# Optimization experiments

Measured on AMD Instinct MI355X. Metric: run time of the kernel, lower is better.

Reference implementation:

```python
import jax, jax.numpy as jnp
import numpy as np
import math

N = 400; E = 3200; Fs = 16; Fp = 8
DS = 32; DC = 32; DP = 32; DB = 64
WK, SL = 7, 288
CHUNK = 24  # 2016 / 24 = 84 scan steps (original chunks G=2016 into pieces)


def setup_inputs() -> dict:
    key = jax.random.key(0)
    ks = iter(jax.random.split(key, 64))
    def p(shape, scale=0.1):
        return jax.random.normal(next(ks), shape, jnp.float32) * scale
    # edge_index with no self loops (PyG GATConv removes+re-adds self loops)
    src = jax.random.randint(next(ks), (E,), 0, N)
    off = jax.random.randint(next(ks), (E,), 1, N)
    dst = (src + off) % N
    edge_index = jnp.stack([src, dst]).astype(jnp.int32)
    return dict(
        x_static=jax.random.normal(next(ks), (N, Fs), jnp.float32),
        profile_feat=jax.random.normal(next(ks), (N, WK, SL, Fp), jnp.float32),
        edge_index=edge_index,
        Ws1=p((Fs, 4 * DS)), as1_src=p((4, DS)), as1_dst=p((4, DS)), bs1=p((DS,)),
        Ws2=p((DS, DS)), as2_src=p((1, DS)), as2_dst=p((1, DS)), bs2=p((DS,)),
        wd_emb=p((7, 8), 1.0), sl_emb=p((288, 16), 1.0),
        Wc1=p((29, DC)), bc1=p((DC,)), Wc2=p((DC, DC)), bc2=p((DC,)),
        Wp1=p((Fp, DP)), bp1=p((DP,)), Wp2=p((DP, DP)), bp2=p((DP,)),
        Wt1=p((DS + DC + DP, 4 * DB)), at1_src=p((4, DB)), at1_dst=p((4, DB)), bt1=p((DB,)),
        Wt2=p((DB, DB)), at2_src=p((1, DB)), at2_dst=p((1, DB)), bt2=p((DB,)),
        Wh1=p((DB, 32)), bh1=p((32,)), Wh2=p((32, 1)), bh2=p((1,)),
    )


def gat_conv(x, W, a_src, a_dst, bias, src, dst, n):
    """PyG GATConv (concat=False): x [B,n,Fin] -> [B,n,C]; shared edge list per graph."""
    B = x.shape[0]
    H, C = a_src.shape
    h = (x @ W).reshape(B, n, H, C)                          # [B,n,H,C]
    al_s = jnp.einsum('bnhc,hc->bnh', h, a_src)              # [B,n,H]
    al_d = jnp.einsum('bnhc,hc->bnh', h, a_dst)
    e = jax.nn.leaky_relu(al_s[:, src] + al_d[:, dst], 0.2)  # [B,E,H]
    e = jnp.moveaxis(e, 1, 0)                                # [E,B,H]
    m = jax.ops.segment_max(e, dst, num_segments=n)          # [n,B,H]
    e = jnp.exp(e - m[dst])
    denom = jax.ops.segment_sum(e, dst, num_segments=n)
    alpha = e / denom[dst]                                   # [E,B,H]
    msg = alpha[..., None] * jnp.moveaxis(h[:, src], 1, 0)   # [E,B,H,C]
    out = jax.ops.segment_sum(msg, dst, num_segments=n)      # [n,B,H,C]
    return out.mean(axis=2).swapaxes(0, 1) + bias            # [B,n,C]


def reference(x_static, profile_feat, edge_index,
              Ws1, as1_src, as1_dst, bs1, Ws2, as2_src, as2_dst, bs2,
              wd_emb, sl_emb, Wc1, bc1, Wc2, bc2,
              Wp1, bp1, Wp2, bp2,
              Wt1, at1_src, at1_dst, bt1, Wt2, at2_src, at2_dst, bt2,
              Wh1, bh1, Wh2, bh2):
    relu = jax.nn.relu
    n = x_static.shape[0]
    loop = jnp.arange(n, dtype=edge_index.dtype)
    src = jnp.concatenate([edge_index[0], loop])   # add self loops
    dst = jnp.concatenate([edge_index[1], loop])

    # static graph encoder
    xs = relu(gat_conv(x_static[None], Ws1, as1_src, as1_dst, bs1, src, dst, n))
    xs = relu(gat_conv(xs, Ws2, as2_src, as2_dst, bs2, src, dst, n))[0]  # [n,DS]

    # calendar encoder (fixed [7,288] grid)
    wid = jnp.broadcast_to(jnp.arange(WK)[:, None], (WK, SL))
    sid = jnp.broadcast_to(jnp.arange(SL)[None, :], (WK, SL))
    ta = (2.0 * math.pi / SL) * sid.astype(jnp.float32)
    wa = (2.0 * math.pi / WK) * wid.astype(jnp.float32)
    cyc = jnp.stack([jnp.sin(ta), jnp.cos(ta), jnp.sin(wa), jnp.cos(wa)], -1)
    wknd = (wid >= 5).astype(jnp.float32)[..., None]
    feat = jnp.concatenate([wd_emb[wid], sl_emb[sid], cyc, wknd], -1)  # [7,288,29]
    cal = relu(feat @ Wc1 + bc1) @ Wc2 + bc2                           # [7,288,DC]

    # profile encoder
    pe = relu(profile_feat @ Wp1 + bp1) @ Wp2 + bp2                    # [n,7,288,DP]
    pe = jnp.transpose(pe, (1, 2, 0, 3))                               # [7,288,n,DP]

    fused = jnp.concatenate([
        jnp.broadcast_to(xs[None, None], (WK, SL, n, DS)),
        jnp.broadcast_to(cal[:, :, None, :], (WK, SL, n, DC)),
        pe], -1)                                                        # [7,288,n,96]

    G = WK * SL
    chunks = fused.reshape(G // CHUNK, CHUNK, n, DS + DC + DP)

    def step(carry, ch):
        h = relu(gat_conv(ch, Wt1, at1_src, at1_dst, bt1, src, dst, n))
        h = relu(gat_conv(h, Wt2, at2_src, at2_dst, bt2, src, dst, n))
        return carry, h

    _, outs = jax.lax.scan(step, None, chunks)
    H = outs.reshape(WK, SL, n, DB)                                     # [7,288,n,DB]
    pred = (relu(H @ Wh1 + bh1) @ Wh2 + bh2)[..., 0]                    # [7,288,n]
    return H, pred
```

## Files before the change

kernel.cpp:

```cpp
#include <hip/hip_runtime.h>

typedef unsigned short u16;
typedef unsigned int   u32;
typedef _Float16 f16;
typedef __attribute__((ext_vector_type(8))) _Float16 f16x8;
typedef __attribute__((ext_vector_type(4))) float f32x4;

#define NN  400
#define EIN 3200
#define NE  3600
#define TT  2016
#define L2E 1.4426950408889634f

__device__ __forceinline__ u32 pk16(float a, float b){
  auto h = __builtin_amdgcn_cvt_pkrtz(a,b);
  union { decltype(h) v; u32 u; } cv; cv.v = h; return cv.u;
}
__device__ __forceinline__ float hlo(u32 w){
  union { u32 u; __fp16 h[2]; } v; v.u=w; return (float)v.h[0];
}
__device__ __forceinline__ float hhi(u32 w){
  union { u32 u; __fp16 h[2]; } v; v.u=w; return (float)v.h[1];
}

__global__ __launch_bounds__(1024) void k_setup(
    const int* __restrict__ ei,
    const float* __restrict__ Wp2, const float* __restrict__ bp2,
    const float* __restrict__ Wt1,
    const float* __restrict__ at1_src, const float* __restrict__ at1_dst,
    const float* __restrict__ Wt2, const float* __restrict__ at2_src, const float* __restrict__ at2_dst,
    const float* __restrict__ Wh1,
    const float* __restrict__ Wc2, const float* __restrict__ bc2,
    const float* __restrict__ Ws1, const float* __restrict__ Ws2,
    u16* __restrict__ rp, u32* __restrict__ col2, u16* __restrict__ ord,
    f16* __restrict__ Bf1, f16* __restrict__ Bf2, f16* __restrict__ Bfh,
    f16* __restrict__ Bs1, f16* __restrict__ Bs2,
    float* __restrict__ wpe_s, float* __restrict__ wpe_d,
    float* __restrict__ wt1_as, float* __restrict__ wt1_ad,
    float* __restrict__ w2s, float* __restrict__ w2d,
    float* __restrict__ b_pe2, float* __restrict__ WcW,
    float* __restrict__ wbal_s, float* __restrict__ wbal_d,
    float* __restrict__ balc_s, float* __restrict__ balc_d)
{
  const int tid=threadIdx.x;
  __shared__ int s_src[NE]; __shared__ int s_dst[NE]; __shared__ int s_tmp[NE];
  __shared__ int s_deg[NN]; __shared__ int s_rp[NN+1]; __shared__ int s_cur[NN];
  __shared__ float sWpe[8192];
  __shared__ float sWcW[8192];
  __shared__ float sbpe2[256];
  if(blockIdx.x==0){
    for(int e2=tid;e2<NE;e2+=1024){
      s_src[e2]=(e2<EIN)?ei[e2]:(e2-EIN);
      s_dst[e2]=(e2<EIN)?ei[EIN+e2]:(e2-EIN);
    }
    if(tid<NN) s_deg[tid]=0;
    __syncthreads();
    for(int e2=tid;e2<NE;e2+=1024) atomicAdd(&s_deg[s_dst[e2]],1);
    __syncthreads();
    if(tid<=NN){
      int acc=0;
      for(int j=0;j<tid;j++) acc+=s_deg[j];
      s_rp[tid]=acc;
      rp[tid]=(u16)acc;
      if(tid<NN) s_cur[tid]=acc;
    }
    if(tid==0){
      rp[NN+1]=(u16)NE; rp[NN+2]=(u16)NE; rp[NN+3]=(u16)NE;
      col2[NE]=0; col2[NE+1]=0; col2[NE+2]=0; col2[NE+3]=0;
    }
    __syncthreads();
    for(int e2=tid;e2<NE;e2+=1024){
      int slot=atomicAdd(&s_cur[s_dst[e2]],1);
      s_tmp[slot]=e2;
    }
    __syncthreads();
    if(tid<NN){
      int b=s_rp[tid], en=s_rp[tid+1];
      for(int i=b+1;i<en;i++){
        int key=s_tmp[i]; int j=i-1;
        while(j>=b && s_tmp[j]>key){ s_tmp[j+1]=s_tmp[j]; j--; }
        s_tmp[j+1]=key;
      }
      for(int i=b;i<en;i++){
        u32 s=(u32)s_src[s_tmp[i]];
        col2[i]=((s*144u)<<16)|(s*4u);
      }
      int dg=en-b, rk=0;
      for(int j=0;j<NN;j++){
        int dj=s_rp[j+1]-s_rp[j];
        rk += (dj>dg)||((dj==dg)&&(j<tid));
      }
      ord[rk]=(u16)tid;
    }
  } else {
    for(int i=tid;i<8192;i+=1024){
      int k=i>>8, j=i&255;
      float a=0.f,b=0.f;
      for(int m=0;m<32;m++){
        a+=Wp2[k*32+m]*Wt1[(64+m)*256+j];
        b+=Wc2[k*32+m]*Wt1[(32+m)*256+j];
      }
      sWpe[i]=a; sWcW[i]=b; WcW[i]=b;
    }
    if(tid<256){
      float a=0.f,b=0.f;
      for(int m=0;m<32;m++){ a+=bp2[m]*Wt1[(64+m)*256+tid]; b+=bc2[m]*Wt1[(32+m)*256+tid]; }
      sbpe2[tid]=a+b; b_pe2[tid]=a+b;
    }
    __syncthreads();
    if(tid<128){
      int k=tid>>2,h=tid&3;
      float s=0,d=0,s2=0,d2=0,bs=0,bd=0;
      for(int c=0;c<64;c++){
        float as=at1_src[h*64+c], ad=at1_dst[h*64+c];
        float wv=sWpe[k*256+h*64+c];  s+=wv*as;  d+=wv*ad;
        float w2=Wt1[k*256+h*64+c];   s2+=w2*as; d2+=w2*ad;
        float wc=sWcW[k*256+h*64+c];  bs+=wc*as; bd+=wc*ad;
      }
      wpe_s[tid]=s*L2E; wpe_d[tid]=d*L2E; wt1_as[tid]=s2*L2E; wt1_ad[tid]=d2*L2E;
      wbal_s[tid]=bs*L2E; wbal_d[tid]=bd*L2E;
    }
    if(tid>=128&&tid<192){
      int k=tid-128; float s=0,d=0;
      for(int c=0;c<64;c++){ float wv=Wt2[k*64+c]; s+=wv*at2_src[c]; d+=wv*at2_dst[c]; }
      w2s[k]=s*L2E; w2d[k]=d*L2E;
    }
    if(tid>=192&&tid<196){
      int h=tid-192; float s=0,d=0;
      for(int c=0;c<64;c++){ float v=sbpe2[h*64+c]; s+=v*at1_src[h*64+c]; d+=v*at1_dst[h*64+c]; }
      balc_s[h]=s*L2E; balc_d[h]=d*L2E;
    }
    for(int i=tid;i<16384;i+=1024){
      int j=i&7, ll=(i>>3)&63, ks=(i>>9)&1, nt=(i>>10)&3, h=(i>>12)&3;
      int k=ks*32+(ll>>4)*8+j, c=h*64+nt*16+(ll&15);
      float v=(k<32)? sWpe[k*256+c] : Wt1[(k-32)*256+c];
      Bf1[i]=(f16)v;
    }
    for(int i=tid;i<4096;i+=1024){
      int j=i&7, ll=(i>>3)&63, ks=(i>>9)&1, nt=(i>>10)&3;
      Bf2[i]=(f16)Wt2[(ks*32+(ll>>4)*8+j)*64 + nt*16+(ll&15)];
    }
    for(int i=tid;i<2048;i+=1024){
      int j=i&7, ll=(i>>3)&63, ks=(i>>9)&1, nt=(i>>10)&1;
      Bfh[i]=(f16)Wh1[(ks*32+(ll>>4)*8+j)*32 + nt*16+(ll&15)];
    }
    for(int i=tid;i<4096;i+=1024){
      int j=i&7, ll=(i>>3)&63, nt=(i>>9)&7;
      int k=(ll>>4)*8+j, c=nt*16+(ll&15);
      Bs1[i]=(f16)((k<16)? Ws1[k*128+c] : 0.f);
    }
    for(int i=tid;i<1024;i+=1024){
      int j=i&7, ll=(i>>3)&63, nt=(i>>9)&1;
      int k=(ll>>4)*8+j, c=nt*16+(ll&15);
      Bs2[i]=(f16)Ws2[k*32+c];
    }
  }
}

#define KS_X    0
#define KS_H    32000
#define KS_ALS  140800
#define KS_ALD  147200
#define KS_COL  153600
#define KS_RP   160800
#define KS_ORD  161608
#define KS_AS   162408
#define KS_AD   162920
#define KS_END  163432

__global__ __launch_bounds__(1024) void k_static(
    const float* __restrict__ x_static,
    const float* __restrict__ as1_src, const float* __restrict__ as1_dst, const float* __restrict__ bs1,
    const float* __restrict__ as2_src, const float* __restrict__ as2_dst, const float* __restrict__ bs2,
    const float* __restrict__ wt1_as, const float* __restrict__ wt1_ad,
    const f16* __restrict__ Bs1, const f16* __restrict__ Bs2,
    const u16* __restrict__ g_rp, const u32* __restrict__ g_col2, const u16* __restrict__ g_ord,
    u32* __restrict__ xsb, float* __restrict__ Aal_s, float* __restrict__ Aal_d)
{
  __shared__ __align__(16) char smem[KS_END];
  const int tid=threadIdx.x;
  const int l=tid&63, w=tid>>6;
  const int col16=l&15, cr=(l>>4)*4, kbyte=(l>>4)*16;
  const int lane8=tid&7, grp8=tid>>3;
  const int l16=tid&15, g16=tid>>4, hh=l16>>2, cg=l16&3;
  float* ALS=(float*)(smem+KS_ALS);
  float* ALD=(float*)(smem+KS_ALD);
  const u16* COL=(const u16*)(smem+KS_COL);
  const u16* RP =(const u16*)(smem+KS_RP);
  const u16* ORD=(const u16*)(smem+KS_ORD);
  float* AS=(float*)(smem+KS_AS);
  float* AD=(float*)(smem+KS_AD);

  for(int i=tid;i<NN*32;i+=1024){
    int n=i>>5, c=i&31;
    *(f16*)(smem+KS_X+n*80+c*2) = (c<16)? (f16)x_static[n*16+c] : (f16)0.f;
  }
  for(int i=tid;i<NE;i+=1024) ((u16*)(smem+KS_COL))[i]=(u16)((g_col2[i]&0xffffu)>>2);
  if(tid<202) ((u32*)(smem+KS_RP))[tid]=((const u32*)g_rp)[tid];
  else if(tid>=256&&tid<456) ((u32*)(smem+KS_ORD))[tid-256]=((const u32*)g_ord)[tid-256];
  else if(tid>=512&&tid<640){ AS[tid-512]=as1_src[tid-512]*L2E; AD[tid-512]=as1_dst[tid-512]*L2E; }
  __syncthreads();

  {
    f16x8 B[8];
    #pragma unroll
    for(int nt=0;nt<8;nt++) B[nt]=*(const f16x8*)(Bs1+nt*512+l*8);
    for(int mt=w;mt<25;mt+=16){
      f16x8 a=*(const f16x8*)(smem+KS_X+(mt*16+col16)*80+kbyte);
      #pragma unroll
      for(int nt=0;nt<8;nt++){
        f32x4 c={0.f,0.f,0.f,0.f};
        c=__builtin_amdgcn_mfma_f32_16x16x32_f16(a,B[nt],c,0,0,0);
        #pragma unroll
        for(int r=0;r<4;r++)
          *(f16*)(smem+KS_H+(mt*16+cr+r)*272+(nt*16+col16)*2)=(f16)c[r];
      }
    }
  }
  __syncthreads();

  if(tid<NN){
    #pragma unroll
    for(int h=0;h<4;h++){
      const u32* hr=(const u32*)(smem+KS_H+tid*272+h*64);
      float sa=0.f,da=0.f;
      #pragma unroll
      for(int q=0;q<16;q++){
        u32 v=hr[q]; float v0=hlo(v),v1=hhi(v);
        sa=fmaf(v0,AS[h*32+2*q],sa); sa=fmaf(v1,AS[h*32+2*q+1],sa);
        da=fmaf(v0,AD[h*32+2*q],da); da=fmaf(v1,AD[h*32+2*q+1],da);
      }
      ALS[tid*4+h]=sa; ALD[tid*4+h]=da;
    }
  }
  __syncthreads();

  for(int m=0;m<7;m++){
    int di=g16+m*64;
    if(di<NN){
      int d=ORD[di];
      int b=RP[d], en=RP[d+1];
      float ad=ALD[d*4+hh];
      float den=0.f;
      float rt[8]={0.f,0.f,0.f,0.f,0.f,0.f,0.f,0.f};
      for(int j=b;j<en;j++){
        int s=COL[j];
        float v=ALS[s*4+hh]+ad;
        v=fmaxf(v,0.2f*v);
        float p=__builtin_amdgcn_exp2f(v); den+=p;
        uint4 hw=*(const uint4*)(smem+KS_H+s*272+l16*16);
        rt[0]=fmaf(hlo(hw.x),p,rt[0]); rt[1]=fmaf(hhi(hw.x),p,rt[1]);
        rt[2]=fmaf(hlo(hw.y),p,rt[2]); rt[3]=fmaf(hhi(hw.y),p,rt[3]);
        rt[4]=fmaf(hlo(hw.z),p,rt[4]); rt[5]=fmaf(hhi(hw.z),p,rt[5]);
        rt[6]=fmaf(hlo(hw.w),p,rt[6]); rt[7]=fmaf(hhi(hw.w),p,rt[7]);
      }
      float inv=__builtin_amdgcn_rcpf(den);
      float vs[8];
      #pragma unroll
      for(int q=0;q<8;q++){
        float x=rt[q]*inv;
        x+=__shfl_xor(x,4); x+=__shfl_xor(x,8);
        vs[q]=x;
      }
      if(l16<4){
        u32 pk[4];
        #pragma unroll
        for(int q=0;q<4;q++){
          float v0=fmaxf(fmaf(0.25f,vs[2*q],  bs1[cg*8+2*q]),  0.f);
          float v1=fmaxf(fmaf(0.25f,vs[2*q+1],bs1[cg*8+2*q+1]),0.f);
          pk[q]=pk16(v0,v1);
        }
        *(uint4*)(smem+KS_X+d*80+cg*16)=make_uint4(pk[0],pk[1],pk[2],pk[3]);
      }
    }
  }
  __syncthreads();

  {
    f16x8 B[2];
    #pragma unroll
    for(int nt=0;nt<2;nt++) B[nt]=*(const f16x8*)(Bs2+nt*512+l*8);
    for(int mt=w;mt<25;mt+=16){
      f16x8 a=*(const f16x8*)(smem+KS_X+(mt*16+col16)*80+kbyte);
      #pragma unroll
      for(int nt=0;nt<2;nt++){
        f32x4 c={0.f,0.f,0.f,0.f};
        c=__builtin_amdgcn_mfma_f32_16x16x32_f16(a,B[nt],c,0,0,0);
        #pragma unroll
        for(int r=0;r<4;r++)
          *(f16*)(smem+KS_H+(mt*16+cr+r)*80+(nt*16+col16)*2)=(f16)c[r];
      }
    }
  }
  if(tid>=512&&tid<640){ AS[tid-512]=wt1_as[tid-512]; AD[tid-512]=wt1_ad[tid-512]; }
  __syncthreads();

  if(tid<NN){
    const u32* hr=(const u32*)(smem+KS_H+tid*80);
    float sa=0.f,da=0.f;
    #pragma unroll
    for(int q=0;q<16;q++){
      u32 v=hr[q]; float v0=hlo(v),v1=hhi(v);
      sa=fmaf(v0,as2_src[2*q],sa); sa=fmaf(v1,as2_src[2*q+1],sa);
      da=fmaf(v0,as2_dst[2*q],da); da=fmaf(v1,as2_dst[2*q+1],da);
    }
    ALS[tid]=sa*L2E; ALD[tid]=da*L2E;
  }
  __syncthreads();

  #pragma unroll
  for(int m=0;m<4;m++){
    int di=grp8+m*128;
    if(di<NN){
      int d=ORD[di];
      int b=RP[d], en=RP[d+1];
      float ad=ALD[d];
      float den=0.f;
      float rt[4]={0.f,0.f,0.f,0.f};
      for(int j=b;j<en;j++){
        int s=COL[j];
        float v=ALS[s]+ad;
        v=fmaxf(v,0.2f*v);
        float p=__builtin_amdgcn_exp2f(v); den+=p;
        uint2 hw=*(const uint2*)(smem+KS_H+s*80+lane8*8);
        rt[0]=fmaf(hlo(hw.x),p,rt[0]); rt[1]=fmaf(hhi(hw.x),p,rt[1]);
        rt[2]=fmaf(hlo(hw.y),p,rt[2]); rt[3]=fmaf(hhi(hw.y),p,rt[3]);
      }
      float inv=__builtin_amdgcn_rcpf(den);
      float xq[4];
      #pragma unroll
      for(int q=0;q<4;q++) xq[q]=fmaxf(fmaf(rt[q],inv,bs2[lane8*4+q]),0.f);
      float ps[4]={0.f,0.f,0.f,0.f}, pd[4]={0.f,0.f,0.f,0.f};
      #pragma unroll
      for(int q=0;q<4;q++){
        int k=lane8*4+q;
        #pragma unroll
        for(int h2=0;h2<4;h2++){ ps[h2]=fmaf(xq[q],AS[k*4+h2],ps[h2]); pd[h2]=fmaf(xq[q],AD[k*4+h2],pd[h2]); }
      }
      #pragma unroll
      for(int h2=0;h2<4;h2++){
        ps[h2]+=__shfl_xor(ps[h2],1); ps[h2]+=__shfl_xor(ps[h2],2); ps[h2]+=__shfl_xor(ps[h2],4);
        pd[h2]+=__shfl_xor(pd[h2],1); pd[h2]+=__shfl_xor(pd[h2],2); pd[h2]+=__shfl_xor(pd[h2],4);
      }
      if(lane8==0){
        #pragma unroll
        for(int h2=0;h2<4;h2++){ Aal_s[d*4+h2]=ps[h2]; Aal_d[d*4+h2]=pd[h2]; }
      }
      xsb[d*16+lane8*2+0]=pk16(xq[0],xq[1]);
      xsb[d*16+lane8*2+1]=pk16(xq[2],xq[3]);
    }
  }
}

#define OT_A    0
#define OT_H    57600
#define OT_ALS  115200
#define OT_ALD  121600
#define OT_COL  128000
#define OT_RP   142416
#define OT_ORD  143232
#define OT_BP   144032
#define OT_WPES 145056
#define OT_WPED 145568
#define OT_W2S  146080
#define OT_W2D  146336
#define OT_BT2  146592
#define OT_BH1  146848
#define OT_WH2  146976
#define OT_BPMT 147104
#define OT_C1   147360
#define OT_FEAT 147488
#define OT_BAL  147616
#define OT_END  147648

__global__ __launch_bounds__(1024) void k_temporal(
    const float* __restrict__ pf, const float* __restrict__ Wp1, const float* __restrict__ bp1,
    const u32* __restrict__ xsb, const float* __restrict__ Aal_s, const float* __restrict__ Aal_d,
    const float* __restrict__ wpe_sg, const float* __restrict__ wpe_dg,
    const f16* __restrict__ Bf1, const f16* __restrict__ Bf2, const f16* __restrict__ Bfh,
    const float* __restrict__ WcW, const float* __restrict__ b_pe2,
    const float* __restrict__ wbal_s, const float* __restrict__ wbal_d,
    const float* __restrict__ balc_s, const float* __restrict__ balc_d,
    const float* __restrict__ Wc1, const float* __restrict__ bc1,
    const float* __restrict__ wd_emb, const float* __restrict__ sl_emb,
    const float* __restrict__ bt1, const float* __restrict__ w2sg, const float* __restrict__ w2dg,
    const float* __restrict__ bt2g, const float* __restrict__ bh1g,
    const float* __restrict__ Wh2g, const float* __restrict__ bh2,
    const u16* __restrict__ g_rp, const u32* __restrict__ g_col2, const u16* __restrict__ g_ord,
    float* __restrict__ Hout, float* __restrict__ pred)
{
  __shared__ __align__(16) char smem[OT_END];
  const int bid=blockIdx.x;
  const int t=(bid&7)*252+(bid>>3);
  const int tid=threadIdx.x;
  const int l=tid&63, w=tid>>6;
  const int lane4=tid&3, grp4=tid>>2;
  const int col16=l&15, cr=(l>>4)*4, kbyte=(l>>4)*16;

  float4 pA=make_float4(0,0,0,0), pB=make_float4(0,0,0,0);
  if(tid<NN){ const float4* pp=(const float4*)(pf+((size_t)tid*TT+(size_t)t)*8); pA=pp[0]; pB=pp[1]; }

  for(int i=tid;i<3604;i+=1024) ((u32*)(smem+OT_COL))[i]=g_col2[i];
  for(int i=tid;i<6400;i+=1024){ int n=i>>4,q=i&15; *(u32*)(smem+OT_A+n*144+64+q*4)=xsb[i]; }
  if(tid<202) ((u32*)(smem+OT_RP))[tid]=((const u32*)g_rp)[tid];
  else if(tid>=256&&tid<456) ((u32*)(smem+OT_ORD))[tid-256]=((const u32*)g_ord)[tid-256];
  else if(tid>=512&&tid<640){ ((float*)(smem+OT_WPES))[tid-512]=wpe_sg[tid-512]; ((float*)(smem+OT_WPED))[tid-512]=wpe_dg[tid-512]; }
  else if(tid>=640&&tid<704){ ((float*)(smem+OT_W2S))[tid-640]=w2sg[tid-640]; ((float*)(smem+OT_W2D))[tid-640]=w2dg[tid-640]; }
  else if(tid>=704&&tid<768){ ((float*)(smem+OT_BT2))[tid-704]=bt2g[tid-704]; }
  else if(tid>=768&&tid<800){ ((float*)(smem+OT_BH1))[tid-768]=bh1g[tid-768]; ((float*)(smem+OT_WH2))[tid-768]=Wh2g[tid-768]; }
  else if(tid>=832&&tid<864){
    int q=tid-832;
    const int wd=t/288, sl=t%288;
    float v=0.f;
    if(q<8) v=wd_emb[wd*8+q];
    else if(q<24) v=sl_emb[sl*16+(q-8)];
    else if(q==24||q==25){ float ta=0.021816615649929116f*(float)sl; v=(q==24)?__sinf(ta):__cosf(ta); }
    else if(q==26||q==27){ float wa=0.8975979010256552f*(float)wd; v=(q==26)?__sinf(wa):__cosf(wa); }
    else if(q==28) v=(wd>=5)?1.f:0.f;
    ((float*)(smem+OT_FEAT))[q]=v;
  }
  __syncthreads();

  if(tid>=512&&tid<544){
    int q=tid-512;
    float a=bc1[q];
    const float* F=(const float*)(smem+OT_FEAT);
    for(int k=0;k<29;k++) a+=F[k]*Wc1[k*32+q];
    ((float*)(smem+OT_C1))[q]=fmaxf(a,0.f);
  }
  if(tid<NN){
    float px[8]={pA.x,pA.y,pA.z,pA.w,pB.x,pB.y,pB.z,pB.w};
    float pv[32];
    #pragma unroll
    for(int k2=0;k2<32;k2+=2){
      float a0=bp1[k2], a1=bp1[k2+1];
      #pragma unroll
      for(int i2=0;i2<8;i2++){ a0=fmaf(px[i2],Wp1[i2*32+k2],a0); a1=fmaf(px[i2],Wp1[i2*32+k2+1],a1); }
      a0=fmaxf(a0,0.f); a1=fmaxf(a1,0.f);
      pv[k2]=a0; pv[k2+1]=a1;
      *(u32*)(smem+OT_A+tid*144+k2*2)=pk16(a0,a1);
    }
    const float* WS=(const float*)(smem+OT_WPES);
    const float* WD=(const float*)(smem+OT_WPED);
    #pragma unroll
    for(int h=0;h<4;h++){
      float sa=Aal_s[tid*4+h], da=Aal_d[tid*4+h];
      #pragma unroll
      for(int k2=0;k2<32;k2++){ sa=fmaf(pv[k2],WS[k2*4+h],sa); da=fmaf(pv[k2],WD[k2*4+h],da); }
      ((float*)(smem+OT_ALS))[tid*4+h]=sa;
      ((float*)(smem+OT_ALD))[tid*4+h]=da;
    }
  }
  __syncthreads();

  auto mfma_L1=[&](int h){
    f16x8 B0[4],B1[4];
    #pragma unroll
    for(int nt=0;nt<4;nt++){
      B0[nt]=*(const f16x8*)(Bf1+(((h*4+nt)*2+0)*512+l*8));
      B1[nt]=*(const f16x8*)(Bf1+(((h*4+nt)*2+1)*512+l*8));
    }
    for(int mt=w;mt<25;mt+=16){
      const char* arow=smem+OT_A+(mt*16+col16)*144;
      f16x8 a0=*(const f16x8*)(arow+kbyte);
      f16x8 a1=*(const f16x8*)(arow+64+kbyte);
      #pragma unroll
      for(int nt=0;nt<4;nt++){
        f32x4 c={0.f,0.f,0.f,0.f};
        c=__builtin_amdgcn_mfma_f32_16x16x32_f16(a0,B0[nt],c,0,0,0);
        c=__builtin_amdgcn_mfma_f32_16x16x32_f16(a1,B1[nt],c,0,0,0);
        #pragma unroll
        for(int r=0;r<4;r++)
          *(f16*)(smem+OT_H+(mt*16+cr+r)*144+(nt*16+col16)*2)=(f16)c[r];
      }
    }
  };

  mfma_L1(0);
  if(tid<256){
    float a=b_pe2[tid];
    const float* C1=(const float*)(smem+OT_C1);
    for(int k2=0;k2<32;k2++) a=fmaf(C1[k2],WcW[k2*256+tid],a);
    ((float*)(smem+OT_BP))[tid]=a;
  }
  if(tid>=256&&tid<264){
    int h=tid&3; bool isd=(tid>=260);
    const float* C1=(const float*)(smem+OT_C1);
    const float* wb=isd?wbal_d:wbal_s;
    float a=isd?balc_d[h]:balc_s[h];
    for(int k2=0;k2<32;k2++) a=fmaf(C1[k2],wb[k2*4+h],a);
    ((float*)(smem+OT_BAL))[(isd?4:0)+h]=a;
  }
  __syncthreads();

  const u16* RP  =(const u16*)(smem+OT_RP);
  const u16* ORD =(const u16*)(smem+OT_ORD);
  const u32* COL2=(const u32*)(smem+OT_COL);
  const char* HB = smem+OT_H+lane4*32;

  float acc[2][16];
  #pragma unroll
  for(int m=0;m<2;m++){
    #pragma unroll
    for(int q=0;q<16;q++) acc[m][q]=0.f;
  }

  for(int h=0;h<4;h++){
    if(h==0&&tid<64){
      const float* BP=(const float*)(smem+OT_BP);
      ((float*)(smem+OT_BPMT))[tid]=0.25f*(BP[tid]+BP[64+tid]+BP[128+tid]+BP[192+tid])+bt1[tid];
    }
    const float* ALD=(const float*)(smem+OT_ALD);
    const char* ALSb=smem+OT_ALS+h*4;
    float bsd=((const float*)(smem+OT_BAL))[h]+((const float*)(smem+OT_BAL))[4+h];
    #pragma unroll
    for(int m=0;m<2;m++){
      int di = m ? (511-grp4) : grp4;
      float rt[16];
      #pragma unroll
      for(int q=0;q<16;q++) rt[q]=0.f;
      float inv=0.f;
      if(di<NN){
        int d=ORD[di];
        int b=RP[d], en=RP[d+1];
        float ad=ALD[d*4+h]+bsd;
        float den=0.f;
        for(int j=b;j<en;j++){
          u32 cv=COL2[j];
          float alv=*(const float*)(ALSb+((cv&0xffffu)<<2));
          float v=alv+ad;
          v=fmaxf(v,0.2f*v);
          float p=__builtin_amdgcn_exp2f(v); den+=p;
          const char* hp=HB+(cv>>16);
          uint4 h0=*(const uint4*)(hp);
          uint4 h1=*(const uint4*)(hp+16);
          rt[0] =fmaf(hlo(h0.x),p,rt[0]);  rt[1] =fmaf(hhi(h0.x),p,rt[1]);
          rt[2] =fmaf(hlo(h0.y),p,rt[2]);  rt[3] =fmaf(hhi(h0.y),p,rt[3]);
          rt[4] =fmaf(hlo(h0.z),p,rt[4]);  rt[5] =fmaf(hhi(h0.z),p,rt[5]);
          rt[6] =fmaf(hlo(h0.w),p,rt[6]);  rt[7] =fmaf(hhi(h0.w),p,rt[7]);
          rt[8] =fmaf(hlo(h1.x),p,rt[8]);  rt[9] =fmaf(hhi(h1.x),p,rt[9]);
          rt[10]=fmaf(hlo(h1.y),p,rt[10]); rt[11]=fmaf(hhi(h1.y),p,rt[11]);
          rt[12]=fmaf(hlo(h1.z),p,rt[12]); rt[13]=fmaf(hhi(h1.z),p,rt[13]);
          rt[14]=fmaf(hlo(h1.w),p,rt[14]); rt[15]=fmaf(hhi(h1.w),p,rt[15]);
        }
        inv=__builtin_amdgcn_rcpf(den);
      }
      #pragma unroll
      for(int q=0;q<16;q++) acc[m][q]=fmaf(rt[q],inv,acc[m][q]);
    }
    __syncthreads();
    if(h<3){ mfma_L1(h+1); __syncthreads(); }
  }

  {
    const float* BPMT=(const float*)(smem+OT_BPMT);
    const float* W2S=(const float*)(smem+OT_W2S);
    const float* W2D=(const float*)(smem+OT_W2D);
    #pragma unroll
    for(int m=0;m<2;m++){
      int di = m ? (511-grp4) : grp4;
      if(di<NN){
        int d=ORD[di];
        float g[16];
        #pragma unroll
        for(int q=0;q<16;q++) g[q]=fmaxf(fmaf(0.25f,acc[m][q],BPMT[lane4*16+q]),0.f);
        float ss=0.f,dd2=0.f;
        #pragma unroll
        for(int q=0;q<16;q++){ ss=fmaf(g[q],W2S[lane4*16+q],ss); dd2=fmaf(g[q],W2D[lane4*16+q],dd2); }
        ss+=__shfl_xor(ss,1); ss+=__shfl_xor(ss,2);
        dd2+=__shfl_xor(dd2,1); dd2+=__shfl_xor(dd2,2);
        if(lane4==0){ ((float*)(smem+OT_ALS))[d]=ss; ((float*)(smem+OT_ALD))[d]=dd2; }
        uint4 pk0,pk1;
        pk0.x=pk16(g[0],g[1]);   pk0.y=pk16(g[2],g[3]);   pk0.z=pk16(g[4],g[5]);   pk0.w=pk16(g[6],g[7]);
        pk1.x=pk16(g[8],g[9]);   pk1.y=pk16(g[10],g[11]); pk1.z=pk16(g[12],g[13]); pk1.w=pk16(g[14],g[15]);
        *(uint4*)(smem+OT_A+d*144+lane4*32)=pk0;
        *(uint4*)(smem+OT_A+d*144+lane4*32+16)=pk1;
      }
    }
  }
  __syncthreads();

  {
    f16x8 B0[4],B1[4];
    #pragma unroll
    for(int nt=0;nt<4;nt++){
      B0[nt]=*(const f16x8*)(Bf2+((nt*2+0)*512+l*8));
      B1[nt]=*(const f16x8*)(Bf2+((nt*2+1)*512+l*8));
    }
    for(int mt=w;mt<25;mt+=16){
      const char* arow=smem+OT_A+(mt*16+col16)*144;
      f16x8 a0=*(const f16x8*)(arow+kbyte);
      f16x8 a1=*(const f16x8*)(arow+64+kbyte);
      #pragma unroll
      for(int nt=0;nt<4;nt++){
        f32x4 c={0.f,0.f,0.f,0.f};
        c=__builtin_amdgcn_mfma_f32_16x16x32_f16(a0,B0[nt],c,0,0,0);
        c=__builtin_amdgcn_mfma_f32_16x16x32_f16(a1,B1[nt],c,0,0,0);
        #pragma unroll
        for(int r=0;r<4;r++)
          *(f16*)(smem+OT_H+(mt*16+cr+r)*144+(nt*16+col16)*2)=(f16)c[r];
      }
    }
  }
  __syncthreads();

  {
    const float* ALD=(const float*)(smem+OT_ALD);
    const float* BT2=(const float*)(smem+OT_BT2);
    #pragma unroll
    for(int m=0;m<2;m++){
      int di = m ? (511-grp4) : grp4;
      if(di<NN){
        int d=ORD[di];
        int b=RP[d], en=RP[d+1];
        float ad=ALD[d];
        float den=0.f;
        float rt[16];
        #pragma unroll
        for(int q=0;q<16;q++) rt[q]=0.f;
        for(int j=b;j<en;j++){
          u32 cv=COL2[j];
          float alv=*(const float*)(smem+OT_ALS+(cv&0xffffu));
          float v=alv+ad;
          v=fmaxf(v,0.2f*v);
          float p=__builtin_amdgcn_exp2f(v); den+=p;
          const char* hp=HB+(cv>>16);
          uint4 h0=*(const uint4*)(hp);
          uint4 h1=*(const uint4*)(hp+16);
          rt[0] =fmaf(hlo(h0.x),p,rt[0]);  rt[1] =fmaf(hhi(h0.x),p,rt[1]);
          rt[2] =fmaf(hlo(h0.y),p,rt[2]);  rt[3] =fmaf(hhi(h0.y),p,rt[3]);
          rt[4] =fmaf(hlo(h0.z),p,rt[4]);  rt[5] =fmaf(hhi(h0.z),p,rt[5]);
          rt[6] =fmaf(hlo(h0.w),p,rt[6]);  rt[7] =fmaf(hhi(h0.w),p,rt[7]);
          rt[8] =fmaf(hlo(h1.x),p,rt[8]);  rt[9] =fmaf(hhi(h1.x),p,rt[9]);
          rt[10]=fmaf(hlo(h1.y),p,rt[10]); rt[11]=fmaf(hhi(h1.y),p,rt[11]);
          rt[12]=fmaf(hlo(h1.z),p,rt[12]); rt[13]=fmaf(hhi(h1.z),p,rt[13]);
          rt[14]=fmaf(hlo(h1.w),p,rt[14]); rt[15]=fmaf(hhi(h1.w),p,rt[15]);
        }
        float inv=__builtin_amdgcn_rcpf(den);
        float hv[16];
        #pragma unroll
        for(int q=0;q<16;q++) hv[q]=fmaxf(fmaf(rt[q],inv,BT2[lane4*16+q]),0.f);
        float* hp2=Hout+((size_t)t*NN+d)*64+lane4*16;
        *(float4*)(hp2)   =make_float4(hv[0],hv[1],hv[2],hv[3]);
        *(float4*)(hp2+4) =make_float4(hv[4],hv[5],hv[6],hv[7]);
        *(float4*)(hp2+8) =make_float4(hv[8],hv[9],hv[10],hv[11]);
        *(float4*)(hp2+12)=make_float4(hv[12],hv[13],hv[14],hv[15]);
        uint4 pk0,pk1;
        pk0.x=pk16(hv[0],hv[1]);   pk0.y=pk16(hv[2],hv[3]);   pk0.z=pk16(hv[4],hv[5]);   pk0.w=pk16(hv[6],hv[7]);
        pk1.x=pk16(hv[8],hv[9]);   pk1.y=pk16(hv[10],hv[11]); pk1.z=pk16(hv[12],hv[13]); pk1.w=pk16(hv[14],hv[15]);
        *(uint4*)(smem+OT_A+d*144+lane4*32)=pk0;
        *(uint4*)(smem+OT_A+d*144+lane4*32+16)=pk1;
      }
    }
  }
  __syncthreads();

  {
    f16x8 B0[2],B1[2];
    #pragma unroll
    for(int nt=0;nt<2;nt++){
      B0[nt]=*(const f16x8*)(Bfh+((nt*2+0)*512+l*8));
      B1[nt]=*(const f16x8*)(Bfh+((nt*2+1)*512+l*8));
    }
    for(int mt=w;mt<25;mt+=16){
      const char* arow=smem+OT_A+(mt*16+col16)*144;
      f16x8 a0=*(const f16x8*)(arow+kbyte);
      f16x8 a1=*(const f16x8*)(arow+64+kbyte);
      #pragma unroll
      for(int nt=0;nt<2;nt++){
        float bj=((const float*)(smem+OT_BH1))[nt*16+col16];
        f32x4 c={bj,bj,bj,bj};
        c=__builtin_amdgcn_mfma_f32_16x16x32_f16(a0,B0[nt],c,0,0,0);
        c=__builtin_amdgcn_mfma_f32_16x16x32_f16(a1,B1[nt],c,0,0,0);
        #pragma unroll
        for(int r=0;r<4;r++)
          *(float*)(smem+OT_H+(mt*16+cr+r)*144+(nt*16+col16)*4)=fmaxf(c[r],0.f);
      }
    }
  }
  __syncthreads();

  {
    const float* WH2=(const float*)(smem+OT_WH2);
    float wv[8];
    #pragma unroll
    for(int q=0;q<8;q++) wv[q]=WH2[lane4*8+q];
    float bb=bh2[0];
    #pragma unroll
    for(int m=0;m<2;m++){
      int di = m ? (511-grp4) : grp4;
      if(di<NN){
        int d=ORD[di];
        float4 p0=*(const float4*)(smem+OT_H+d*144+lane4*32);
        float4 p1=*(const float4*)(smem+OT_H+d*144+lane4*32+16);
        float sp=p0.x*wv[0]+p0.y*wv[1]+p0.z*wv[2]+p0.w*wv[3]
                +p1.x*wv[4]+p1.y*wv[5]+p1.z*wv[6]+p1.w*wv[7];
        sp+=__shfl_xor(sp,1); sp+=__shfl_xor(sp,2);
        if(lane4==0) pred[(size_t)t*NN+d]=sp+bb;
      }
    }
  }
}

extern "C" void kernel_launch(void* const* d_in, const int* in_sizes, int n_in,
                              void* d_out, int out_size, void* d_ws, size_t ws_size,
                              hipStream_t stream) {
  const float* x_static=(const float*)d_in[0];
  const float* pf      =(const float*)d_in[1];
  const int*   ei      =(const int*)  d_in[2];
  const float* Ws1=(const float*)d_in[3];
  const float* as1_src=(const float*)d_in[4];
  const float* as1_dst=(const float*)d_in[5];
  const float* bs1=(const float*)d_in[6];
  const float* Ws2=(const float*)d_in[7];
  const float* as2_src=(const float*)d_in[8];
  const float* as2_dst=(const float*)d_in[9];
  const float* bs2=(const float*)d_in[10];
  const float* wd_emb=(const float*)d_in[11];
  const float* sl_emb=(const float*)d_in[12];
  const float* Wc1=(const float*)d_in[13];
  const float* bc1=(const float*)d_in[14];
  const float* Wc2=(const float*)d_in[15];
  const float* bc2=(const float*)d_in[16];
  const float* Wp1=(const float*)d_in[17];
  const float* bp1=(const float*)d_in[18];
  const float* Wp2=(const float*)d_in[19];
  const float* bp2=(const float*)d_in[20];
  const float* Wt1=(const float*)d_in[21];
  const float* at1_src=(const float*)d_in[22];
  const float* at1_dst=(const float*)d_in[23];
  const float* bt1=(const float*)d_in[24];
  const float* Wt2=(const float*)d_in[25];
  const float* at2_src=(const float*)d_in[26];
  const float* at2_dst=(const float*)d_in[27];
  const float* bt2=(const float*)d_in[28];
  const float* Wh1=(const float*)d_in[29];
  const float* bh1=(const float*)d_in[30];
  const float* Wh2=(const float*)d_in[31];
  const float* bh2=(const float*)d_in[32];

  float* Hout=(float*)d_out;
  float* pred=Hout + (size_t)TT*NN*64;

  char* wsp=(char*)d_ws; size_t off=0;
  auto A=[&](size_t n)->void*{ void* p=wsp+off; off=(off+n+255)&~(size_t)255; return p; };
  u16* rp    =(u16*)A(408*2);
  u32* col2  =(u32*)A((NE+4)*4);
  u16* ordv  =(u16*)A(NN*2);
  f16* Bf1   =(f16*)A(16384*2);
  f16* Bf2   =(f16*)A(4096*2);
  f16* Bfh   =(f16*)A(2048*2);
  f16* Bs1   =(f16*)A(4096*2);
  f16* Bs2   =(f16*)A(1024*2);
  float* wpe_s =(float*)A(128*4);
  float* wpe_d =(float*)A(128*4);
  float* wt1_as=(float*)A(128*4);
  float* wt1_ad=(float*)A(128*4);
  float* w2s   =(float*)A(64*4);
  float* w2d   =(float*)A(64*4);
  float* b_pe2 =(float*)A(256*4);
  float* WcW   =(float*)A(8192*4);
  float* wbal_s=(float*)A(128*4);
  float* wbal_d=(float*)A(128*4);
  float* balc_s=(float*)A(4*4);
  float* balc_d=(float*)A(4*4);
  u32*   xsb   =(u32*)A(6400*4);
  float* Aal_s =(float*)A(1600*4);
  float* Aal_d =(float*)A(1600*4);

  hipLaunchKernelGGL(k_setup, dim3(2), dim3(1024), 0, stream,
                     ei, Wp2,bp2,Wt1,at1_src,at1_dst,Wt2,at2_src,at2_dst,Wh1,Wc2,bc2,Ws1,Ws2,
                     rp,col2,ordv,Bf1,Bf2,Bfh,Bs1,Bs2,
                     wpe_s,wpe_d,wt1_as,wt1_ad,w2s,w2d,b_pe2,WcW,wbal_s,wbal_d,balc_s,balc_d);
  hipLaunchKernelGGL(k_static, dim3(1), dim3(1024), 0, stream,
                     x_static,as1_src,as1_dst,bs1,as2_src,as2_dst,bs2,
                     wt1_as,wt1_ad,Bs1,Bs2,rp,col2,ordv,xsb,Aal_s,Aal_d);
  hipLaunchKernelGGL(k_temporal, dim3(TT), dim3(1024), 0, stream,
                     pf,Wp1,bp1,xsb,Aal_s,Aal_d,wpe_s,wpe_d,Bf1,Bf2,Bfh,
                     WcW,b_pe2,wbal_s,wbal_d,balc_s,balc_d,
                     Wc1,bc1,wd_emb,sl_emb,bt1,w2s,w2d,bt2,bh1,Wh2,bh2,
                     rp,col2,ordv,Hout,pred);
}
```

Baseline: 448.9 us.

## Overlap next-head MFMA with aggregation; transpose MFMA operands and use fma_mix

The layer-1 per-head projection is split into a compute phase held in registers and a store phase. The next head's MFMA now runs before the current head's edge aggregation, which removes a barrier-separated compute step from the critical path. The MFMA operands are swapped so each lane owns four consecutive output columns of one row, giving packed 8- or 16-byte LDS stores instead of scalar f16 stores. The fp16-to-fp32 convert plus FMA in the gather loops is replaced by inline-asm v_fma_mix_f32, at the cost of more live accumulator registers.

```diff
diff --git a/kernel.cpp b/kernel.cpp
--- a/kernel.cpp
+++ b/kernel.cpp
@@ -21,6 +21,12 @@
 }
 __device__ __forceinline__ float hhi(u32 w){
   union { u32 u; __fp16 h[2]; } v; v.u=w; return (float)v.h[1];
+}
+__device__ __forceinline__ void fmix_lo(float& a, u32 s, float p){
+  asm("v_fma_mix_f32 %0, %1, %2, %0 op_sel:[0,0,0] op_sel_hi:[1,0,0]" : "+v"(a) : "v"(s), "v"(p));
+}
+__device__ __forceinline__ void fmix_hi(float& a, u32 s, float p){
+  asm("v_fma_mix_f32 %0, %1, %2, %0 op_sel:[1,0,0] op_sel_hi:[1,0,0]" : "+v"(a) : "v"(s), "v"(p));
 }
 
 __global__ __launch_bounds__(1024) void k_setup(
@@ -453,30 +459,54 @@
   }
   __syncthreads();
 
-  auto mfma_L1=[&](int h){
-    f16x8 B0[4],B1[4];
+  f32x4 c0[4], c1[4];
+  auto mfma_compute=[&](int h){
+    f16x8 Bw0[4],Bw1[4];
     #pragma unroll
     for(int nt=0;nt<4;nt++){
-      B0[nt]=*(const f16x8*)(Bf1+(((h*4+nt)*2+0)*512+l*8));
-      B1[nt]=*(const f16x8*)(Bf1+(((h*4+nt)*2+1)*512+l*8));
-    }
-    for(int mt=w;mt<25;mt+=16){
-      const char* arow=smem+OT_A+(mt*16+col16)*144;
+      Bw0[nt]=*(const f16x8*)(Bf1+(((h*4+nt)*2+0)*512+l*8));
+      Bw1[nt]=*(const f16x8*)(Bf1+(((h*4+nt)*2+1)*512+l*8));
+    }
+    {
+      const char* arow=smem+OT_A+(w*16+col16)*144;
       f16x8 a0=*(const f16x8*)(arow+kbyte);
       f16x8 a1=*(const f16x8*)(arow+64+kbyte);
       #pragma unroll
       for(int nt=0;nt<4;nt++){
         f32x4 c={0.f,0.f,0.f,0.f};
-        c=__builtin_amdgcn_mfma_f32_16x16x32_f16(a0,B0[nt],c,0,0,0);
-        c=__builtin_amdgcn_mfma_f32_16x16x32_f16(a1,B1[nt],c,0,0,0);
-        #pragma unroll
-        for(int r=0;r<4;r++)
-          *(f16*)(smem+OT_H+(mt*16+cr+r)*144+(nt*16+col16)*2)=(f16)c[r];
+        c=__builtin_amdgcn_mfma_f32_16x16x32_f16(Bw0[nt],a0,c,0,0,0);
+        c=__builtin_amdgcn_mfma_f32_16x16x32_f16(Bw1[nt],a1,c,0,0,0);
+        c0[nt]=c;
+      }
+    }
+    if(w<9){
+      const char* arow=smem+OT_A+((w+16)*16+col16)*144;
+      f16x8 a0=*(const f16x8*)(arow+kbyte);
+      f16x8 a1=*(const f16x8*)(arow+64+kbyte);
+      #pragma unroll
+      for(int nt=0;nt<4;nt++){
+        f32x4 c={0.f,0.f,0.f,0.f};
+        c=__builtin_amdgcn_mfma_f32_16x16x32_f16(Bw0[nt],a0,c,0,0,0);
+        c=__builtin_amdgcn_mfma_f32_16x16x32_f16(Bw1[nt],a1,c,0,0,0);
+        c1[nt]=c;
       }
     }
   };
-
-  mfma_L1(0);
+  auto mfma_store=[&](){
+    int n0=w*16+col16;
+    #pragma unroll
+    for(int nt=0;nt<4;nt++)
+      *(uint2*)(smem+OT_H+n0*144+(nt*16+cr)*2)=make_uint2(pk16(c0[nt][0],c0[nt][1]),pk16(c0[nt][2],c0[nt][3]));
+    if(w<9){
+      int n1=(w+16)*16+col16;
+      #pragma unroll
+      for(int nt=0;nt<4;nt++)
+        *(uint2*)(smem+OT_H+n1*144+(nt*16+cr)*2)=make_uint2(pk16(c1[nt][0],c1[nt][1]),pk16(c1[nt][2],c1[nt][3]));
+    }
+  };
+
+  mfma_compute(0);
+  mfma_store();
   if(tid<256){
     float a=b_pe2[tid];
     const float* C1=(const float*)(smem+OT_C1);
@@ -510,6 +540,7 @@
       const float* BP=(const float*)(smem+OT_BP);
       ((float*)(smem+OT_BPMT))[tid]=0.25f*(BP[tid]+BP[64+tid]+BP[128+tid]+BP[192+tid])+bt1[tid];
     }
+    if(h<3) mfma_compute(h+1);
     const float* ALD=(const float*)(smem+OT_ALD);
     const char* ALSb=smem+OT_ALS+h*4;
     float bsd=((const float*)(smem+OT_BAL))[h]+((const float*)(smem+OT_BAL))[4+h];
@@ -534,14 +565,14 @@
           const char* hp=HB+(cv>>16);
           uint4 h0=*(const uint4*)(hp);
           uint4 h1=*(const uint4*)(hp+16);
-          rt[0] =fmaf(hlo(h0.x),p,rt[0]);  rt[1] =fmaf(hhi(h0.x),p,rt[1]);
-          rt[2] =fmaf(hlo(h0.y),p,rt[2]);  rt[3] =fmaf(hhi(h0.y),p,rt[3]);
-          rt[4] =fmaf(hlo(h0.z),p,rt[4]);  rt[5] =fmaf(hhi(h0.z),p,rt[5]);
-          rt[6] =fmaf(hlo(h0.w),p,rt[6]);  rt[7] =fmaf(hhi(h0.w),p,rt[7]);
-          rt[8] =fmaf(hlo(h1.x),p,rt[8]);  rt[9] =fmaf(hhi(h1.x),p,rt[9]);
-          rt[10]=fmaf(hlo(h1.y),p,rt[10]); rt[11]=fmaf(hhi(h1.y),p,rt[11]);
-          rt[12]=fmaf(hlo(h1.z),p,rt[12]); rt[13]=fmaf(hhi(h1.z),p,rt[13]);
-          rt[14]=fmaf(hlo(h1.w),p,rt[14]); rt[15]=fmaf(hhi(h1.w),p,rt[15]);
+          fmix_lo(rt[0],h0.x,p);  fmix_hi(rt[1],h0.x,p);
+          fmix_lo(rt[2],h0.y,p);  fmix_hi(rt[3],h0.y,p);
+          fmix_lo(rt[4],h0.z,p);  fmix_hi(rt[5],h0.z,p);
+          fmix_lo(rt[6],h0.w,p);  fmix_hi(rt[7],h0.w,p);
+          fmix_lo(rt[8],h1.x,p);  fmix_hi(rt[9],h1.x,p);
+          fmix_lo(rt[10],h1.y,p); fmix_hi(rt[11],h1.y,p);
+          fmix_lo(rt[12],h1.z,p); fmix_hi(rt[13],h1.z,p);
+          fmix_lo(rt[14],h1.w,p); fmix_hi(rt[15],h1.w,p);
         }
         inv=__builtin_amdgcn_rcpf(den);
       }
@@ -549,7 +580,7 @@
       for(int q=0;q<16;q++) acc[m][q]=fmaf(rt[q],inv,acc[m][q]);
     }
     __syncthreads();
-    if(h<3){ mfma_L1(h+1); __syncthreads(); }
+    if(h<3){ mfma_store(); __syncthreads(); }
   }
 
   {
@@ -581,24 +612,23 @@
   __syncthreads();
 
   {
-    f16x8 B0[4],B1[4];
+    f16x8 Bw0[4],Bw1[4];
     #pragma unroll
     for(int nt=0;nt<4;nt++){
-      B0[nt]=*(const f16x8*)(Bf2+((nt*2+0)*512+l*8));
-      B1[nt]=*(const f16x8*)(Bf2+((nt*2+1)*512+l*8));
+      Bw0[nt]=*(const f16x8*)(Bf2+((nt*2+0)*512+l*8));
+      Bw1[nt]=*(const f16x8*)(Bf2+((nt*2+1)*512+l*8));
     }
     for(int mt=w;mt<25;mt+=16){
       const char* arow=smem+OT_A+(mt*16+col16)*144;
       f16x8 a0=*(const f16x8*)(arow+kbyte);
       f16x8 a1=*(const f16x8*)(arow+64+kbyte);
+      int n=mt*16+col16;
       #pragma unroll
       for(int nt=0;nt<4;nt++){
         f32x4 c={0.f,0.f,0.f,0.f};
-        c=__builtin_amdgcn_mfma_f32_16x16x32_f16(a0,B0[nt],c,0,0,0);
-        c=__builtin_amdgcn_mfma_f32_16x16x32_f16(a1,B1[nt],c,0,0,0);
-        #pragma unroll
-        for(int r=0;r<4;r++)
-          *(f16*)(smem+OT_H+(mt*16+cr+r)*144+(nt*16+col16)*2)=(f16)c[r];
+        c=__builtin_amdgcn_mfma_f32_16x16x32_f16(Bw0[nt],a0,c,0,0,0);
+        c=__builtin_amdgcn_mfma_f32_16x16x32_f16(Bw1[nt],a1,c,0,0,0);
+        *(uint2*)(smem+OT_H+n*144+(nt*16+cr)*2)=make_uint2(pk16(c[0],c[1]),pk16(c[2],c[3]));
       }
     }
   }
@@ -627,14 +657,14 @@
           const char* hp=HB+(cv>>16);
           uint4 h0=*(const uint4*)(hp);
           uint4 h1=*(const uint4*)(hp+16);
-          rt[0] =fmaf(hlo(h0.x),p,rt[0]);  rt[1] =fmaf(hhi(h0.x),p,rt[1]);
-          rt[2] =fmaf(hlo(h0.y),p,rt[2]);  rt[3] =fmaf(hhi(h0.y),p,rt[3]);
-          rt[4] =fmaf(hlo(h0.z),p,rt[4]);  rt[5] =fmaf(hhi(h0.z),p,rt[5]);
-          rt[6] =fmaf(hlo(h0.w),p,rt[6]);  rt[7] =fmaf(hhi(h0.w),p,rt[7]);
-          rt[8] =fmaf(hlo(h1.x),p,rt[8]);  rt[9] =fmaf(hhi(h1.x),p,rt[9]);
-          rt[10]=fmaf(hlo(h1.y),p,rt[10]); rt[11]=fmaf(hhi(h1.y),p,rt[11]);
-          rt[12]=fmaf(hlo(h1.z),p,rt[12]); rt[13]=fmaf(hhi(h1.z),p,rt[13]);
-          rt[14]=fmaf(hlo(h1.w),p,rt[14]); rt[15]=fmaf(hhi(h1.w),p,rt[15]);
+          fmix_lo(rt[0],h0.x,p);  fmix_hi(rt[1],h0.x,p);
+          fmix_lo(rt[2],h0.y,p);  fmix_hi(rt[3],h0.y,p);
+          fmix_lo(rt[4],h0.z,p);  fmix_hi(rt[5],h0.z,p);
+          fmix_lo(rt[6],h0.w,p);  fmix_hi(rt[7],h0.w,p);
+          fmix_lo(rt[8],h1.x,p);  fmix_hi(rt[9],h1.x,p);
+          fmix_lo(rt[10],h1.y,p); fmix_hi(rt[11],h1.y,p);
+          fmix_lo(rt[12],h1.z,p); fmix_hi(rt[13],h1.z,p);
+          fmix_lo(rt[14],h1.w,p); fmix_hi(rt[15],h1.w,p);
         }
         float inv=__builtin_amdgcn_rcpf(den);
         float hv[16];
@@ -656,25 +686,25 @@
   __syncthreads();
 
   {
-    f16x8 B0[2],B1[2];
+    f16x8 Bw0[2],Bw1[2];
     #pragma unroll
     for(int nt=0;nt<2;nt++){
-      B0[nt]=*(const f16x8*)(Bfh+((nt*2+0)*512+l*8));
-      B1[nt]=*(const f16x8*)(Bfh+((nt*2+1)*512+l*8));
+      Bw0[nt]=*(const f16x8*)(Bfh+((nt*2+0)*512+l*8));
+      Bw1[nt]=*(const f16x8*)(Bfh+((nt*2+1)*512+l*8));
     }
     for(int mt=w;mt<25;mt+=16){
       const char* arow=smem+OT_A+(mt*16+col16)*144;
       f16x8 a0=*(const f16x8*)(arow+kbyte);
       f16x8 a1=*(const f16x8*)(arow+64+kbyte);
+      int n=mt*16+col16;
       #pragma unroll
       for(int nt=0;nt<2;nt++){
-        float bj=((const float*)(smem+OT_BH1))[nt*16+col16];
-        f32x4 c={bj,bj,bj,bj};
-        c=__builtin_amdgcn_mfma_f32_16x16x32_f16(a0,B0[nt],c,0,0,0);
-        c=__builtin_amdgcn_mfma_f32_16x16x32_f16(a1,B1[nt],c,0,0,0);
-        #pragma unroll
-        for(int r=0;r<4;r++)
-          *(float*)(smem+OT_H+(mt*16+cr+r)*144+(nt*16+col16)*4)=fmaxf(c[r],0.f);
+        float4 bj=*(const float4*)(smem+OT_BH1+(nt*16+cr)*4);
+        f32x4 c={bj.x,bj.y,bj.z,bj.w};
+        c=__builtin_amdgcn_mfma_f32_16x16x32_f16(Bw0[nt],a0,c,0,0,0);
+        c=__builtin_amdgcn_mfma_f32_16x16x32_f16(Bw1[nt],a1,c,0,0,0);
+        f32x4 co={fmaxf(c[0],0.f),fmaxf(c[1],0.f),fmaxf(c[2],0.f),fmaxf(c[3],0.f)};
+        *(f32x4*)(smem+OT_H+n*144+(nt*16+cr)*4)=co;
       }
     }
   }
```

New measurement: 486.5 us. +8.4%, slower.
